# Kernel optimization log

Hardware: AMD Instinct MI355X
Metric: run time of the kernel (lower is better)

## Reference

```python
import jax, jax.numpy as jnp
import numpy as np

C = 64  # num_channels
B, H, W = 16, 160, 160


def squeeze2d(x, f=2):
    b, c, h, w = x.shape
    x = x.reshape(b, c, h // f, f, w // f, f)
    x = x.transpose(0, 1, 3, 5, 2, 4)
    return x.reshape(b, c * f * f, h // f, w // f)


def unsqueeze2d(x, f=2):
    b, c, h, w = x.shape
    x = x.reshape(b, c // (f * f), f, f, h, w)
    x = x.transpose(0, 1, 4, 2, 5, 3)
    return x.reshape(b, c // (f * f), h * f, w * f)


def get_indices(num_channels):
    # generate_ind(p) tiles the row-major-flattened 2x2 pattern over C//4 channel groups
    def gen(p):
        return np.tile(np.array(p, dtype=bool), num_channels // 4)
    m = np.ones(num_channels, dtype=bool)
    t = gen([0, 0, 1, 1]); b = ~t
    l = gen([0, 1, 0, 1]); r = ~l
    return (m, t, b, l, r, t & l, t & r, b & l, b & r)


INDS = get_indices(C)


def conv1x1(z, w):
    # 1x1 conv == channel matmul
    return jnp.einsum('oc,bchw->bohw', w, z)


def partition_input(x):
    z = unsqueeze2d(x)
    z = jnp.pad(z, ((0, 0), (0, 0), (1, 1), (1, 1)), constant_values=-1.0)
    z = squeeze2d(z)  # (B, C, H+1, W+1)
    m, t, b, l, r, tl, tr, bl, br = INDS
    return (z[:, :, 1:-1, 1:-1],
            z[:, t, :1, 1:-1], z[:, b, -1:, 1:-1],
            z[:, l, 1:-1, :1], z[:, r, 1:-1, -1:],
            z[:, tl, :1, :1], z[:, tr, :1, -1:],
            z[:, bl, -1:, :1], z[:, br, -1:, -1:])


def unsqueeze_line(ze):
    b, c = ze.shape[:2]
    sz = (1, -1) if ze.shape[-2] == 1 else (-1, 1)
    return ze.reshape(b, c // 2, 2, -1).transpose(0, 1, 3, 2).reshape(b, c // 2, *sz)


def merge_output(z_m, z_t, z_b, z_l, z_r, z_tl, z_tr, z_bl, z_br):
    z_m = unsqueeze2d(z_m)
    z_t, z_b, z_l, z_r = [unsqueeze_line(zi) for zi in (z_t, z_b, z_l, z_r)]
    z_tt = jnp.concatenate([z_tl, z_t, z_tr], axis=3)
    z_mm = jnp.concatenate([z_l, z_m, z_r], axis=3)
    z_bb = jnp.concatenate([z_bl, z_b, z_br], axis=3)
    return squeeze2d(jnp.concatenate([z_tt, z_mm, z_bb], axis=2))


def setup_inputs() -> dict:
    key = jax.random.key(0)
    k1, k2 = jax.random.split(key)
    x = jax.random.normal(k1, (B, C, H, W), dtype=jnp.float32)
    logdet = jax.random.normal(k2, (B,), dtype=jnp.float32)
    rng = np.random.RandomState(0)
    w_init = np.linalg.qr(rng.randn(C, C))[0].astype(np.float32)
    weight = jnp.asarray(w_init)
    return {"input": x, "logdet": logdet, "weight": weight}


def reference(input, logdet, weight):
    h, w = input.shape[-2:]
    pixels = [(h - 1) * (w - 1), w - 1, w - 1, h - 1, h - 1, 1, 1, 1, 1]
    ws = [weight[np.ix_(ind, ind)] for ind in INDS]
    dlogdet = sum(jnp.linalg.slogdet(wi)[1] * p for wi, p in zip(ws, pixels))
    zs = partition_input(input)
    outs = [conv1x1(z, wi) for z, wi in zip(zs, ws)]
    output = merge_output(*outs)
    return output, logdet + dlogdet
```

## Files before the change

kernel.cpp:

```cpp
#include <hip/hip_runtime.h>
#include <math.h>

#define NB 16
#define NC 64
#define HW 160
#define PLANE (HW * HW)
#define SG 161
#define NSITES (NB * SG * SG)
#define NCONVBLK ((NSITES + 63) / 64)
#define OUT_LD_OFF (NB * NC * PLANE)

__device__ inline int chmap(int i, int n, int pa, int pb) {
    if (n == 64) return i;
    if (n == 32) return ((i >> 1) << 2) | ((i & 1) ? pb : pa);
    return (i << 2) | pa;
}

__device__ float wave_lu_logabsdet(const float* __restrict__ W, float* A,
                                   int n, int sh, int pa, int pb, int lane) {
    for (int e = lane; e < n * n; e += 64) {
        int i = e >> sh, j = e & (n - 1);
        A[e] = W[chmap(i, n, pa, pb) * 64 + chmap(j, n, pa, pb)];
    }
    asm volatile("s_waitcnt lgkmcnt(0) vmcnt(0)" ::: "memory");
    float logdet = 0.f;
    for (int k = 0; k < n; ++k) {
        float cand = -1.f;
        int idx = k;
        if (lane >= k && lane < n) {
            cand = fabsf(A[(lane << sh) + k]);
            idx = lane;
        }
        for (int off = 32; off; off >>= 1) {
            float oc = __shfl_down(cand, off, 64);
            int oi = __shfl_down(idx, off, 64);
            if (oc > cand) { cand = oc; idx = oi; }
        }
        int p = __shfl(idx, 0, 64);
        if (p != k && lane < n) {
            float tk = A[(k << sh) + lane];
            float tp = A[(p << sh) + lane];
            A[(k << sh) + lane] = tp;
            A[(p << sh) + lane] = tk;
        }
        asm volatile("s_waitcnt lgkmcnt(0)" ::: "memory");
        float piv = A[(k << sh) + k];
        logdet += logf(fabsf(piv));
        float rpiv = 1.f / piv;
        float ckj = (lane < n) ? A[(k << sh) + lane] : 0.f;
        bool act = (lane > k) && (lane < n);
        for (int i2 = k + 1; i2 < n; ++i2) {
            float aik = A[(i2 << sh) + k];
            float mult = aik * rpiv;
            if (act) A[(i2 << sh) + lane] = fmaf(-mult, ckj, A[(i2 << sh) + lane]);
        }
        asm volatile("s_waitcnt lgkmcnt(0)" ::: "memory");
    }
    return logdet;
}

__global__ __launch_bounds__(256, 6) void InvConv1x1GridAlign_kernel(
    const float* __restrict__ x, const float* __restrict__ ld_in,
    const float* __restrict__ W, float* __restrict__ out) {
    __shared__ float A64[64 * 64];
    __shared__ float A32a[32 * 32];
    __shared__ float A32b[32 * 32];
    __shared__ float A16[16 * 16];
    __shared__ float partial[4];

    if (blockIdx.x == 0) {
        int wid = threadIdx.x >> 6;
        int lane = threadIdx.x & 63;
        float part = 0.f;
        if (wid == 0) {
            part = 25281.f * wave_lu_logabsdet(W, A64, 64, 6, 0, 0, lane);
        } else if (wid == 1) {
            part  = wave_lu_logabsdet(W, A32a, 32, 5, 2, 3, lane);
            part += wave_lu_logabsdet(W, A32a, 32, 5, 0, 1, lane);
            part *= 159.f;
        } else if (wid == 2) {
            part  = wave_lu_logabsdet(W, A32b, 32, 5, 1, 3, lane);
            part += wave_lu_logabsdet(W, A32b, 32, 5, 0, 2, lane);
            part *= 159.f;
        } else {
            part  = wave_lu_logabsdet(W, A16, 16, 4, 3, 0, lane);
            part += wave_lu_logabsdet(W, A16, 16, 4, 2, 0, lane);
            part += wave_lu_logabsdet(W, A16, 16, 4, 1, 0, lane);
            part += wave_lu_logabsdet(W, A16, 16, 4, 0, 0, lane);
        }
        if (lane == 0) partial[wid] = part;
        __syncthreads();
        if (threadIdx.x < NB) {
            float dl = partial[0] + partial[1] + partial[2] + partial[3];
            out[OUT_LD_OFF + threadIdx.x] = ld_in[threadIdx.x] + dl;
        }
        return;
    }

    int w = threadIdx.x >> 6;
    int l = threadIdx.x & 63;
    int s = (blockIdx.x - 1) * 64 + l;
    bool live = s < NSITES;
    int sc = live ? s : 0;
    unsigned us = (unsigned)sc;
    unsigned b = us / (SG * SG);
    unsigned rr = us - b * (SG * SG);
    unsigned uy = rr / SG;
    int Y = (int)uy;
    int X = (int)(rr - uy * SG);

    const float* xb = x + (size_t)b * NC * PLANE;
    float* ob = out + (size_t)b * NC * PLANE;

    bool okT = (Y >= 1), okB = (Y <= HW - 1), okL = (X >= 1), okR = (X <= HW - 1);
    bool v00 = live && okT && okL, v01 = live && okT && okR;
    bool v10 = live && okB && okL, v11 = live && okB && okR;
    int off00 = (Y - 1) * HW + (X - 1);
    int off01 = (Y - 1) * HW + X;
    int off10 = Y * HW + (X - 1);
    int off11 = Y * HW + X;

    {
        const float* xw = xb + (size_t)w * 16 * PLANE;
        float* Arow = A64 + w * 16 * 64 + l;
#pragma unroll
        for (int g = 0; g < 4; ++g) {
            const float* pg = xw + (size_t)g * 4 * PLANE;
            Arow[(g * 4 + 0) * 64] = v00 ? pg[3 * PLANE + off00] : 0.f;
            Arow[(g * 4 + 1) * 64] = v01 ? pg[2 * PLANE + off01] : 0.f;
            Arow[(g * 4 + 2) * 64] = v10 ? pg[1 * PLANE + off10] : 0.f;
            Arow[(g * 4 + 3) * 64] = v11 ? pg[0 * PLANE + off11] : 0.f;
        }
    }
    __syncthreads();

    int wu = __builtin_amdgcn_readfirstlane(w);
    const float* Wbase = W + (size_t)wu * 16 * 64;
    float u[16];
#pragma unroll
    for (int j = 0; j < 16; ++j) u[j] = 0.f;

#pragma unroll
    for (int cb = 0; cb < 4; ++cb) {
        float v[16];
#pragma unroll
        for (int i = 0; i < 16; ++i) v[i] = A64[(cb * 16 + i) * 64 + l];
#pragma unroll
        for (int j = 0; j < 16; ++j) {
            const float* wr = Wbase + j * 64 + cb * 16;
            float a = u[j];
#pragma unroll
            for (int k = 0; k < 16; ++k) a = fmaf(wr[k], v[k], a);
            u[j] = a;
        }
    }

    {
        float* ow = ob + (size_t)w * 16 * PLANE;
#pragma unroll
        for (int g = 0; g < 4; ++g) {
            float* pg = ow + (size_t)g * 4 * PLANE;
            if (v00) pg[3 * PLANE + off00] = u[g * 4 + 0];
            if (v01) pg[2 * PLANE + off01] = u[g * 4 + 1];
            if (v10) pg[1 * PLANE + off10] = u[g * 4 + 2];
            if (v11) pg[0 * PLANE + off11] = u[g * 4 + 3];
        }
    }
}

extern "C" void kernel_launch(void* const* d_in, const int* in_sizes, int n_in,
                              void* d_out, int out_size, void* d_ws, size_t ws_size,
                              hipStream_t stream) {
    const float* x = (const float*)d_in[0];
    const float* ld = (const float*)d_in[1];
    const float* W = (const float*)d_in[2];
    float* out = (float*)d_out;
    hipLaunchKernelGGL(InvConv1x1GridAlign_kernel, dim3(NCONVBLK + 1), dim3(256), 0,
                       stream, x, ld, W, out);
}
```

Baseline: 294.3 us.

## Parallelize 64x64 LU across block, pad LDS strides, and swizzle block-to-site mapping

Measured after the change: 444.2 us. 50.9% more time.

```diff
diff --git a/kernel.cpp b/kernel.cpp
--- a/kernel.cpp
+++ b/kernel.cpp
@@ -8,6 +8,8 @@
 #define SG 161
 #define NSITES (NB * SG * SG)
 #define NCONVBLK ((NSITES + 63) / 64)
+#define CHUNK ((NCONVBLK + 7) / 8)
+#define PADBLK (8 * CHUNK)
 #define OUT_LD_OFF (NB * NC * PLANE)
 
 __device__ inline int chmap(int i, int n, int pa, int pb) {
@@ -16,79 +18,113 @@
     return (i << 2) | pa;
 }
 
-__device__ float wave_lu_logabsdet(const float* __restrict__ W, float* A,
-                                   int n, int sh, int pa, int pb, int lane) {
+__device__ inline void wave_argmax(float& cand, int& idx) {
+    for (int off = 32; off; off >>= 1) {
+        float oc = __shfl_down(cand, off, 64);
+        int oi = __shfl_down(idx, off, 64);
+        if (oc > cand) { cand = oc; idx = oi; }
+    }
+    idx = __shfl(idx, 0, 64);
+}
+
+__device__ float wave_lu(const float* __restrict__ W, float* A, int n, int sh,
+                         int st, int pa, int pb, int lane) {
     for (int e = lane; e < n * n; e += 64) {
         int i = e >> sh, j = e & (n - 1);
-        A[e] = W[chmap(i, n, pa, pb) * 64 + chmap(j, n, pa, pb)];
+        A[i * st + j] = W[chmap(i, n, pa, pb) * 64 + chmap(j, n, pa, pb)];
     }
     asm volatile("s_waitcnt lgkmcnt(0) vmcnt(0)" ::: "memory");
     float logdet = 0.f;
+    bool colact = lane < n;
     for (int k = 0; k < n; ++k) {
         float cand = -1.f;
         int idx = k;
-        if (lane >= k && lane < n) {
-            cand = fabsf(A[(lane << sh) + k]);
-            idx = lane;
-        }
-        for (int off = 32; off; off >>= 1) {
-            float oc = __shfl_down(cand, off, 64);
-            int oi = __shfl_down(idx, off, 64);
-            if (oc > cand) { cand = oc; idx = oi; }
-        }
-        int p = __shfl(idx, 0, 64);
-        if (p != k && lane < n) {
-            float tk = A[(k << sh) + lane];
-            float tp = A[(p << sh) + lane];
-            A[(k << sh) + lane] = tp;
-            A[(p << sh) + lane] = tk;
+        if (lane >= k && lane < n) { cand = fabsf(A[lane * st + k]); idx = lane; }
+        wave_argmax(cand, idx);
+        int p = idx;
+        float pr = 0.f;
+        if (colact) {
+            float tk = A[k * st + lane], tp = A[p * st + lane];
+            if (p != k) { A[k * st + lane] = tp; A[p * st + lane] = tk; }
+            pr = (p != k) ? tp : tk;
         }
         asm volatile("s_waitcnt lgkmcnt(0)" ::: "memory");
-        float piv = A[(k << sh) + k];
-        logdet += logf(fabsf(piv));
-        float rpiv = 1.f / piv;
-        float ckj = (lane < n) ? A[(k << sh) + lane] : 0.f;
-        bool act = (lane > k) && (lane < n);
-        for (int i2 = k + 1; i2 < n; ++i2) {
-            float aik = A[(i2 << sh) + k];
+        float pivv = __shfl(pr, k, 64);
+        logdet += logf(fabsf(pivv));
+        float rpiv = 1.f / pivv;
+        for (int i = k + 1; i < n; ++i) {
+            float aik = A[i * st + k];
             float mult = aik * rpiv;
-            if (act) A[(i2 << sh) + lane] = fmaf(-mult, ckj, A[(i2 << sh) + lane]);
+            if (colact) A[i * st + lane] = fmaf(-mult, pr, A[i * st + lane]);
         }
         asm volatile("s_waitcnt lgkmcnt(0)" ::: "memory");
     }
     return logdet;
 }
 
-__global__ __launch_bounds__(256, 6) void InvConv1x1GridAlign_kernel(
+__device__ float block_lu64(const float* __restrict__ W, float* A, float* comm,
+                            int wid, int lane) {
+    int tid = wid * 64 + lane;
+    for (int e = tid; e < 64 * 64; e += 256) A[(e >> 6) * 65 + (e & 63)] = W[e];
+    __syncthreads();
+    float logdet = 0.f;
+    for (int k = 0; k < 64; ++k) {
+        if (wid == 0) {
+            float cand = -1.f;
+            int idx = k;
+            if (lane >= k) { cand = fabsf(A[lane * 65 + k]); idx = lane; }
+            wave_argmax(cand, idx);
+            int p = idx;
+            float tk = A[k * 65 + lane], tp = A[p * 65 + lane];
+            if (p != k) { A[k * 65 + lane] = tp; A[p * 65 + lane] = tk; }
+            float prk = (p != k) ? tp : tk;
+            float pivv = __shfl(prk, k, 64);
+            logdet += logf(fabsf(pivv));
+            if (lane == 0) comm[0] = 1.f / pivv;
+        }
+        __syncthreads();
+        float rpiv = comm[0];
+        float pr = A[k * 65 + lane];
+        int i0 = (k + 1) + ((wid - (k + 1)) & 3);
+        for (int i = i0; i < 64; i += 4) {
+            float aik = A[i * 65 + k];
+            float mult = aik * rpiv;
+            A[i * 65 + lane] = fmaf(-mult, pr, A[i * 65 + lane]);
+        }
+        __syncthreads();
+    }
+    return logdet;
+}
+
+__global__ __launch_bounds__(256, 8) void InvConv1x1GridAlign_kernel(
     const float* __restrict__ x, const float* __restrict__ ld_in,
     const float* __restrict__ W, float* __restrict__ out) {
-    __shared__ float A64[64 * 64];
-    __shared__ float A32a[32 * 32];
-    __shared__ float A32b[32 * 32];
-    __shared__ float A16[16 * 16];
+    __shared__ float S[4 * 32 * 33];
+    __shared__ float comm[1];
     __shared__ float partial[4];
 
+    int wid = threadIdx.x >> 6;
+    int l = threadIdx.x & 63;
+
     if (blockIdx.x == 0) {
-        int wid = threadIdx.x >> 6;
-        int lane = threadIdx.x & 63;
-        float part = 0.f;
+        float ld64 = block_lu64(W, S, comm, wid, l);
+        __syncthreads();
+        float* strip = S + wid * 1056;
+        float part;
         if (wid == 0) {
-            part = 25281.f * wave_lu_logabsdet(W, A64, 64, 6, 0, 0, lane);
+            part = 25281.f * ld64 + 159.f * wave_lu(W, strip, 32, 5, 33, 2, 3, l)
+                 + wave_lu(W, strip, 16, 4, 17, 3, 0, l);
         } else if (wid == 1) {
-            part  = wave_lu_logabsdet(W, A32a, 32, 5, 2, 3, lane);
-            part += wave_lu_logabsdet(W, A32a, 32, 5, 0, 1, lane);
-            part *= 159.f;
+            part = 159.f * wave_lu(W, strip, 32, 5, 33, 0, 1, l)
+                 + wave_lu(W, strip, 16, 4, 17, 2, 0, l);
         } else if (wid == 2) {
-            part  = wave_lu_logabsdet(W, A32b, 32, 5, 1, 3, lane);
-            part += wave_lu_logabsdet(W, A32b, 32, 5, 0, 2, lane);
-            part *= 159.f;
+            part = 159.f * wave_lu(W, strip, 32, 5, 33, 1, 3, l)
+                 + wave_lu(W, strip, 16, 4, 17, 1, 0, l);
         } else {
-            part  = wave_lu_logabsdet(W, A16, 16, 4, 3, 0, lane);
-            part += wave_lu_logabsdet(W, A16, 16, 4, 2, 0, lane);
-            part += wave_lu_logabsdet(W, A16, 16, 4, 1, 0, lane);
-            part += wave_lu_logabsdet(W, A16, 16, 4, 0, 0, lane);
-        }
-        if (lane == 0) partial[wid] = part;
+            part = 159.f * wave_lu(W, strip, 32, 5, 33, 0, 2, l)
+                 + wave_lu(W, strip, 16, 4, 17, 0, 0, l);
+        }
+        if (l == 0) partial[wid] = part;
         __syncthreads();
         if (threadIdx.x < NB) {
             float dl = partial[0] + partial[1] + partial[2] + partial[3];
@@ -97,20 +133,22 @@
         return;
     }
 
-    int w = threadIdx.x >> 6;
-    int l = threadIdx.x & 63;
-    int s = (blockIdx.x - 1) * 64 + l;
+    int b0 = blockIdx.x - 1;
+    int sb = (b0 & 7) * CHUNK + (b0 >> 3);
+    if (sb >= NCONVBLK) return;
+
+    int s = sb * 64 + l;
     bool live = s < NSITES;
     int sc = live ? s : 0;
     unsigned us = (unsigned)sc;
-    unsigned b = us / (SG * SG);
-    unsigned rr = us - b * (SG * SG);
+    unsigned bb = us / (SG * SG);
+    unsigned rr = us - bb * (SG * SG);
     unsigned uy = rr / SG;
     int Y = (int)uy;
     int X = (int)(rr - uy * SG);
 
-    const float* xb = x + (size_t)b * NC * PLANE;
-    float* ob = out + (size_t)b * NC * PLANE;
+    const float* xb = x + (size_t)bb * NC * PLANE;
+    float* ob = out + (size_t)bb * NC * PLANE;
 
     bool okT = (Y >= 1), okB = (Y <= HW - 1), okL = (X >= 1), okR = (X <= HW - 1);
     bool v00 = live && okT && okL, v01 = live && okT && okR;
@@ -121,8 +159,8 @@
     int off11 = Y * HW + X;
 
     {
-        const float* xw = xb + (size_t)w * 16 * PLANE;
-        float* Arow = A64 + w * 16 * 64 + l;
+        const float* xw = xb + (size_t)wid * 16 * PLANE;
+        float* Arow = S + wid * 16 * 64 + l;
 #pragma unroll
         for (int g = 0; g < 4; ++g) {
             const float* pg = xw + (size_t)g * 4 * PLANE;
@@ -134,7 +172,7 @@
     }
     __syncthreads();
 
-    int wu = __builtin_amdgcn_readfirstlane(w);
+    int wu = __builtin_amdgcn_readfirstlane(wid);
     const float* Wbase = W + (size_t)wu * 16 * 64;
     float u[16];
 #pragma unroll
@@ -144,7 +182,7 @@
     for (int cb = 0; cb < 4; ++cb) {
         float v[16];
 #pragma unroll
-        for (int i = 0; i < 16; ++i) v[i] = A64[(cb * 16 + i) * 64 + l];
+        for (int i = 0; i < 16; ++i) v[i] = S[(cb * 16 + i) * 64 + l];
 #pragma unroll
         for (int j = 0; j < 16; ++j) {
             const float* wr = Wbase + j * 64 + cb * 16;
@@ -156,7 +194,7 @@
     }
 
     {
-        float* ow = ob + (size_t)w * 16 * PLANE;
+        float* ow = ob + (size_t)wid * 16 * PLANE;
 #pragma unroll
         for (int g = 0; g < 4; ++g) {
             float* pg = ow + (size_t)g * 4 * PLANE;
@@ -175,6 +213,6 @@
     const float* ld = (const float*)d_in[1];
     const float* W = (const float*)d_in[2];
     float* out = (float*)d_out;
-    hipLaunchKernelGGL(InvConv1x1GridAlign_kernel, dim3(NCONVBLK + 1), dim3(256), 0,
+    hipLaunchKernelGGL(InvConv1x1GridAlign_kernel, dim3(PADBLK + 1), dim3(256), 0,
                        stream, x, ld, W, out);
 }
```
